# Optimization experiments

Measured on AMD Instinct MI355X. Metric: run time of the kernel, lower is better.

The kernel has to match this reference:

```python
import jax, jax.numpy as jnp
import numpy as np

B, N, C, K, T = 64, 1024, 256, 512, 64
D_THRESH = 0.5
POWER_ITERS = 20


def _pdist(x):
    # x: [..., K, 3] -> pairwise euclidean distances [..., K, K]
    n = jnp.sum(x * x, axis=-1)
    sq = n[..., :, None] + n[..., None, :] - 2.0 * jnp.einsum('...kc,...lc->...kl', x, x)
    return jnp.sqrt(jnp.maximum(sq, 0.0) + 1e-12)


def _forward(rt, rt_centroids, rt_cls_attn, shift_and_scale, W_in, b_in, W1, b1, W2, b2,
             num_rt, anc_idx, pos_idx, neg_idx):
    valid = jnp.arange(N)[None, :] < num_rt[:, None]                      # [B,N]
    # Normalize.batch_unnormalize: pts * scale + shift on valid tokens
    shift = shift_and_scale[:, None, :3]
    scale = shift_and_scale[:, None, 3:4]
    cent = jnp.where(valid[..., None], rt_centroids * scale + shift, rt_centroids)
    attn = jnp.where(valid, rt_cls_attn, -1e9)
    _, top_idx = jax.lax.top_k(attn, K)                                   # [B,K]
    cent_k = jnp.take_along_axis(cent, top_idx[..., None], axis=1)        # [B,K,3]
    rt_k = jnp.take_along_axis(rt, top_idx[..., None], axis=1)            # [B,K,C]
    # SGV padding mask [T,2,K,K]: rows masked by anchor count, cols by pos/neg counts
    n_eff = jnp.minimum(num_rt, K)
    r = jnp.arange(K)
    row_mask = r[None, :] < n_eff[anc_idx][:, None]                       # [T,K]
    col_mask = jnp.stack([r[None, :] < n_eff[pos_idx][:, None],
                          r[None, :] < n_eff[neg_idx][:, None]], axis=1)  # [T,2,K]
    mask = row_mask[:, None, :, None] & col_mask[:, :, None, :]           # [T,2,K,K]
    # input_linear on anchor / neighbour relay tokens
    anc_f = rt_k[anc_idx] @ W_in + b_in                                   # [T,K,C]
    nn_f = jnp.stack([rt_k[pos_idx], rt_k[neg_idx]], axis=1) @ W_in + b_in  # [T,2,K,C]
    anc_c = cent_k[anc_idx]                                               # [T,K,3]
    nn_c = jnp.stack([cent_k[pos_idx], cent_k[neg_idx]], axis=1)          # [T,2,K,3]
    # feature-space nearest-neighbour correspondences anc -> nn (SpectralGV style)
    fd = (jnp.sum(anc_f ** 2, -1)[:, None, :, None]
          + jnp.sum(nn_f ** 2, -1)[:, :, None, :]
          - 2.0 * jnp.einsum('tkc,tnlc->tnkl', anc_f, nn_f))              # [T,2,K,K]
    corr = jnp.argmin(fd, axis=-1)                                        # [T,2,K]
    q_c = jnp.take_along_axis(nn_c, corr[..., None], axis=2)              # [T,2,K,3]
    q_f = jnp.take_along_axis(nn_f, corr[..., None], axis=2)              # [T,2,K,C]
    # correspondence confidence from feature cosine similarity
    cos = jnp.sum(anc_f[:, None] * q_f, -1) / (
        jnp.linalg.norm(anc_f, axis=-1)[:, None] * jnp.linalg.norm(q_f, axis=-1) + 1e-8)
    s = jax.nn.relu(cos)                                                  # [T,2,K]
    # threshold-masked geometric consistency adjacency
    d_p = _pdist(anc_c)[:, None]                                          # [T,1,K,K]
    d_q = _pdist(q_c)                                                     # [T,2,K,K]
    geo = (jnp.abs(d_p - d_q) < D_THRESH) & mask & (~jnp.eye(K, dtype=bool))
    A = geo.astype(jnp.float32) * s[..., :, None] * s[..., None, :]       # [T,2,K,K]
    # leading eigenvector via power iteration (A is entrywise nonnegative)
    v = jnp.full((T, 2, K), 1.0 / np.sqrt(K), dtype=jnp.float32)
    for _ in range(POWER_ITERS):
        w = jnp.einsum('tnkl,tnl->tnk', A, v)
        v = w / (jnp.linalg.norm(w, axis=-1, keepdims=True) + 1e-8)
    eig = -jnp.sort(-v, axis=-1)                                          # sort_eigvec, descending
    h = jax.nn.relu(eig @ W1 + b1)
    scores = jax.nn.sigmoid(h @ W2 + b2)                                  # [T,2,1]
    targets = jnp.zeros_like(scores).at[:, 0].set(1.0)
    return scores, targets


def setup_inputs() -> dict:
    key = jax.random.key(0)
    ks = jax.random.split(key, 12)
    return {
        'rt': jax.random.normal(ks[0], (B, N, C), jnp.float32),
        'rt_centroids': jax.random.normal(ks[1], (B, N, 3), jnp.float32),
        'rt_cls_attn': jax.random.uniform(ks[2], (B, N), jnp.float32),
        'shift_and_scale': jax.random.uniform(ks[3], (B, 4), jnp.float32),
        'num_rt': jax.random.randint(ks[4], (B,), 128, N, jnp.int32),
        'anc_idx': jax.random.randint(ks[5], (T,), 0, B, jnp.int32),
        'pos_idx': jax.random.randint(ks[6], (T,), 0, B, jnp.int32),
        'neg_idx': jax.random.randint(ks[7], (T,), 0, B, jnp.int32),
        'W_in': jax.random.normal(ks[8], (C, C), jnp.float32) / np.sqrt(C),
        'b_in': jnp.zeros((C,), jnp.float32),
        'W1': jax.random.normal(ks[9], (K, K), jnp.float32) / np.sqrt(K),
        'b1': jnp.zeros((K,), jnp.float32),
        'W2': jax.random.normal(ks[10], (K, 1), jnp.float32) / np.sqrt(K),
        'b2': jnp.zeros((1,), jnp.float32),
    }


def reference(rt, rt_centroids, rt_cls_attn, shift_and_scale, num_rt, anc_idx, pos_idx, neg_idx,
              W_in, b_in, W1, b1, W2, b2):
    return _forward(rt, rt_centroids, rt_cls_attn, shift_and_scale, W_in, b_in, W1, b1, W2, b2,
                    num_rt, anc_idx, pos_idx, neg_idx)
```

## Files before the change

### kernel.cpp

```cpp
#include <hip/hip_runtime.h>
#include <cstddef>

#define BB 64
#define NN 1024
#define CC 256
#define KK 512
#define TT 64
#define NPAIR 128

typedef _Float16 h8 __attribute__((ext_vector_type(8)));
typedef _Float16 h4 __attribute__((ext_vector_type(4)));
typedef float f4 __attribute__((ext_vector_type(4)));

typedef __attribute__((address_space(1))) const void GV;
typedef __attribute__((address_space(3))) void LV;
#define GLDS16(g, s) __builtin_amdgcn_global_load_lds((GV*)(const void*)(g), (LV*)(void*)(s), 16, 0, 0)


__global__ __launch_bounds__(256) void wtrans_kernel(
    const float* __restrict__ Win, _Float16* __restrict__ wth, _Float16* __restrict__ wtl)
{
    __shared__ float t[64][65];
    const int k0 = blockIdx.x * 64, n0 = blockIdx.y * 64;
    const int tid = threadIdx.x;
    const int c = tid & 63, r0 = tid >> 6;
    for (int r = r0; r < 64; r += 4)
        t[r][c] = Win[(size_t)(k0 + r) * CC + n0 + c];
    __syncthreads();
    for (int r = r0; r < 64; r += 4) {
        float x = t[c][r];
        _Float16 h = (_Float16)x;
        size_t o = (size_t)(n0 + r) * CC + k0 + c;
        wth[o] = h;
        wtl[o] = (_Float16)(x - (float)h);
    }
}

__global__ __launch_bounds__(512) void sel_kernel(
    const float* __restrict__ attn, const float* __restrict__ cents,
    const float* __restrict__ sas, const int* __restrict__ num_rt,
    int* __restrict__ topidx, int* __restrict__ neff, float* __restrict__ centk)
{
    __shared__ unsigned long long keys[1024];
    const int b = blockIdx.x, tid = threadIdx.x;
    const int nr = num_rt[b];
    for (int i = tid; i < 1024; i += 512) {
        float a = (i < nr) ? attn[b * NN + i] : -1e9f;
        unsigned u = __float_as_uint(a);
        u = (u & 0x80000000u) ? ~u : (u | 0x80000000u);
        keys[i] = ((unsigned long long)u << 32) | (unsigned)(0xFFFFFFFFu - (unsigned)i);
    }
    __syncthreads();
    for (int k = 2; k <= 1024; k <<= 1) {
        for (int j = k >> 1; j > 0; j >>= 1) {
            int i = ((tid & ~(j - 1)) << 1) | (tid & (j - 1));
            int p = i | j;
            unsigned long long a = keys[i], c = keys[p];
            bool up = (i & k) == 0;
            if (up ? (a < c) : (a > c)) { keys[i] = c; keys[p] = a; }
            __syncthreads();
        }
    }
    {
        unsigned long long key = keys[tid];
        int idx = (int)(~(unsigned)key);
        float x = cents[(b * NN + idx) * 3 + 0];
        float y = cents[(b * NN + idx) * 3 + 1];
        float z = cents[(b * NN + idx) * 3 + 2];
        if (idx < nr) {
            float sc = sas[b * 4 + 3];
            x = x * sc + sas[b * 4 + 0];
            y = y * sc + sas[b * 4 + 1];
            z = z * sc + sas[b * 4 + 2];
        }
        float nc = x * x + y * y + z * z;
        ((float4*)centk)[b * KK + tid] = make_float4(x, y, z, nc);
        topidx[b * KK + tid] = idx;
    }
    if (tid == 0) neff[b] = (nr < KK) ? nr : KK;
}

__global__ __launch_bounds__(256) void feat_mfma(
    const float* __restrict__ rt, const int* __restrict__ topidx,
    const _Float16* __restrict__ wth, const _Float16* __restrict__ wtl,
    const float* __restrict__ bin,
    _Float16* __restrict__ feath, _Float16* __restrict__ featl)
{
    const int mtile = blockIdx.x, nt = blockIdx.y;
    __shared__ _Float16 Ah[128][32], Al[128][32], Bh[128][32], Bl[128][32];
    __shared__ int tix[128];
    const int tid = threadIdx.x;
    const int w = tid >> 6, lane = tid & 63;
    const int quad = lane >> 4, l16 = lane & 15;
    const int wm = (w >> 1) * 64, wl = (w & 1) * 64;
    const int b = mtile >> 2;
    if (tid < 128) tix[tid] = topidx[mtile * 128 + tid];
    __syncthreads();
    const int arow_i = tid >> 1;
    const int aseg = (tid & 1) * 16;
    const float* arow = rt + ((size_t)b * NN + tix[arow_i]) * CC + aseg;
    _Float16* bsh = (w < 2) ? &Bh[0][0] : &Bl[0][0];
    const _Float16* bplane = (w < 2) ? wth : wtl;
    const int rowi = lane >> 2, chunk = lane & 3;

    f4 acc[4][4];
    #pragma unroll
    for (int i = 0; i < 4; i++)
        #pragma unroll
        for (int j = 0; j < 4; j++)
            acc[i][j] = (f4){0.f, 0.f, 0.f, 0.f};

    for (int k0 = 0; k0 < CC; k0 += 32) {
        __syncthreads();
        #pragma unroll
        for (int jj = 0; jj < 4; jj++) {
            int j = (w & 1) * 4 + jj;
            int row = j * 16 + rowi;
            GLDS16(bplane + (size_t)(nt * 128 + row) * CC + k0 + chunk * 8, bsh + j * 512);
        }
        {
            const float4* src = (const float4*)(arow + k0);
            #pragma unroll
            for (int c = 0; c < 2; c++) {
                float4 p = src[2 * c], q2 = src[2 * c + 1];
                float xv[8] = {p.x, p.y, p.z, p.w, q2.x, q2.y, q2.z, q2.w};
                h8 hv, lv;
                #pragma unroll
                for (int j = 0; j < 8; j++) {
                    _Float16 h = (_Float16)xv[j];
                    hv[j] = h;
                    lv[j] = (_Float16)(xv[j] - (float)h);
                }
                *(h8*)&Ah[arow_i][aseg + c * 8] = hv;
                *(h8*)&Al[arow_i][aseg + c * 8] = lv;
            }
        }
        __syncthreads();
        h8 afh[4], afl[4], bfh[4], bfl[4];
        #pragma unroll
        for (int i = 0; i < 4; i++) {
            int ra = wm + i * 16 + l16;
            int rb = wl + i * 16 + l16;
            afh[i] = *(const h8*)&Ah[ra][quad * 8];
            afl[i] = *(const h8*)&Al[ra][quad * 8];
            bfh[i] = *(const h8*)&Bh[rb][quad * 8];
            bfl[i] = *(const h8*)&Bl[rb][quad * 8];
        }
        #pragma unroll
        for (int i = 0; i < 4; i++)
            #pragma unroll
            for (int j = 0; j < 4; j++) {
                acc[i][j] = __builtin_amdgcn_mfma_f32_16x16x32_f16(afh[i], bfh[j], acc[i][j], 0, 0, 0);
                acc[i][j] = __builtin_amdgcn_mfma_f32_16x16x32_f16(afh[i], bfl[j], acc[i][j], 0, 0, 0);
                acc[i][j] = __builtin_amdgcn_mfma_f32_16x16x32_f16(afl[i], bfh[j], acc[i][j], 0, 0, 0);
            }
    }
    #pragma unroll
    for (int j = 0; j < 4; j++) {
        int col = wl + j * 16 + l16;
        float bj = bin[nt * 128 + col];
        #pragma unroll
        for (int i = 0; i < 4; i++)
            #pragma unroll
            for (int r = 0; r < 4; r++) {
                int row = wm + i * 16 + quad * 4 + r;
                float v = acc[i][j][r] + bj;
                _Float16 h = (_Float16)v;
                size_t o = (size_t)(mtile * 128 + row) * CC + nt * 128 + col;
                feath[o] = h;
                featl[o] = (_Float16)(v - (float)h);
            }
    }
}

__global__ __launch_bounds__(256) void norm_kernel(
    const _Float16* __restrict__ feath, const _Float16* __restrict__ featl,
    float* __restrict__ normF)
{
    int r = blockIdx.x * 4 + (threadIdx.x >> 6);
    int lane = threadIdx.x & 63;
    h4 hv = ((const h4*)(feath + (size_t)r * CC))[lane];
    h4 lv = ((const h4*)(featl + (size_t)r * CC))[lane];
    float s = 0.f;
    #pragma unroll
    for (int j = 0; j < 4; j++) {
        float x = (float)hv[j] + (float)lv[j];
        s += x * x;
    }
    for (int off = 32; off; off >>= 1) s += __shfl_down(s, off);
    if (lane == 0) normF[r] = s;
}

__global__ __launch_bounds__(512) void argmin_mfma(
    const _Float16* __restrict__ feath, const _Float16* __restrict__ featl,
    const float* __restrict__ normF,
    const int* __restrict__ anc, const int* __restrict__ pos, const int* __restrict__ neg,
    float* __restrict__ partv, int* __restrict__ partl, float* __restrict__ partd)
{
    const int id = blockIdx.x;
    const int xcd = id & 7, kgrp = id >> 3;
    const int pr = xcd * 16 + (kgrp >> 2);
    const int s = kgrp & 3;
    const int lt = s & 1, kt = s >> 1;
    const int t = pr >> 1, nn2 = pr & 1;
    const int a = anc[t];
    const int bb = nn2 ? neg[t] : pos[t];
    const size_t Abase = ((size_t)a * KK + kt * 256) * CC;
    const size_t Bbase = ((size_t)bb * KK + lt * 256) * CC;
    __shared__ _Float16 S[2][4][8192];
    __shared__ float rdv[256][2];
    __shared__ int   rdl[256][2];
    __shared__ float rdd[256][2];
    const int tid = threadIdx.x;
    const int w = tid >> 6, lane = tid & 63;
    const int quad = lane >> 4, l16 = lane & 15;
    const int wr = w >> 1, wc = w & 1;
    const int rowi = lane >> 2, chunk = lane & 3;
    const int plane = w >> 1;
    const int srow = (w & 1) * 128;
    const _Float16* gsrc = (plane == 0) ? feath + Abase
                         : (plane == 1) ? featl + Abase
                         : (plane == 2) ? feath + Bbase
                         :                featl + Bbase;
    const _Float16* grow = gsrc + (size_t)(srow + rowi) * CC + chunk * 8;

    f4 acc[4][8];
    #pragma unroll
    for (int i = 0; i < 4; i++)
        #pragma unroll
        for (int j = 0; j < 8; j++)
            acc[i][j] = (f4){0.f, 0.f, 0.f, 0.f};

    #pragma unroll
    for (int j = 0; j < 8; j++)
        GLDS16(grow + (size_t)(j * 16) * CC, &S[0][plane][srow * 32 + j * 512]);

    #pragma unroll
    for (int kk = 0; kk < 8; kk++) {
        const int cb = kk & 1;
        if (kk < 7) {
            const int k1 = (kk + 1) * 32;
            #pragma unroll
            for (int j = 0; j < 8; j++)
                GLDS16(grow + (size_t)(j * 16) * CC + k1, &S[cb ^ 1][plane][srow * 32 + j * 512]);
            asm volatile("s_waitcnt vmcnt(8)" ::: "memory");
        } else {
            asm volatile("s_waitcnt vmcnt(0)" ::: "memory");
        }
        __builtin_amdgcn_s_barrier();
        h8 afh[4], afl[4];
        #pragma unroll
        for (int i = 0; i < 4; i++) {
            int ra = wr * 64 + i * 16 + l16;
            afh[i] = *(const h8*)&S[cb][0][ra * 32 + quad * 8];
            afl[i] = *(const h8*)&S[cb][1][ra * 32 + quad * 8];
        }
        #pragma unroll
        for (int j = 0; j < 8; j++) {
            int rb = wc * 128 + j * 16 + l16;
            h8 bfh = *(const h8*)&S[cb][2][rb * 32 + quad * 8];
            h8 bfl = *(const h8*)&S[cb][3][rb * 32 + quad * 8];
            #pragma unroll
            for (int i = 0; i < 4; i++) {
                acc[i][j] = __builtin_amdgcn_mfma_f32_16x16x32_f16(afh[i], bfh, acc[i][j], 0, 0, 0);
                acc[i][j] = __builtin_amdgcn_mfma_f32_16x16x32_f16(afh[i], bfl, acc[i][j], 0, 0, 0);
                acc[i][j] = __builtin_amdgcn_mfma_f32_16x16x32_f16(afl[i], bfh, acc[i][j], 0, 0, 0);
            }
        }
        __builtin_amdgcn_sched_barrier(0);
        __builtin_amdgcn_s_barrier();
    }
    float nbj[8];
    #pragma unroll
    for (int j = 0; j < 8; j++)
        nbj[j] = normF[(size_t)bb * KK + lt * 256 + wc * 128 + j * 16 + l16];
    #pragma unroll
    for (int i = 0; i < 4; i++) {
        #pragma unroll
        for (int r = 0; r < 4; r++) {
            float bv = INFINITY; int bl = 0; float bd = 0.f;
            #pragma unroll
            for (int j = 0; j < 8; j++) {
                float d = acc[i][j][r];
                float v = nbj[j] - 2.f * d;
                int l = lt * 256 + wc * 128 + j * 16 + l16;
                if (v < bv) { bv = v; bl = l; bd = d; }
            }
            #pragma unroll
            for (int off = 1; off < 16; off <<= 1) {
                float ov = __shfl_xor(bv, off);
                int   ol = __shfl_xor(bl, off);
                float od = __shfl_xor(bd, off);
                if (ov < bv || (ov == bv && ol < bl)) { bv = ov; bl = ol; bd = od; }
            }
            if (l16 == 0) {
                int row = wr * 64 + i * 16 + quad * 4 + r;
                rdv[row][wc] = bv;
                rdl[row][wc] = bl;
                rdd[row][wc] = bd;
            }
        }
    }
    __syncthreads();
    if (tid < 256) {
        float bv = rdv[tid][0]; int bl = rdl[tid][0]; float bd = rdd[tid][0];
        float v1 = rdv[tid][1]; int l1 = rdl[tid][1];
        if (v1 < bv || (v1 == bv && l1 < bl)) { bv = v1; bl = l1; bd = rdd[tid][1]; }
        size_t idx = ((size_t)pr * KK + kt * 256 + tid) * 2 + lt;
        partv[idx] = bv; partl[idx] = bl; partd[idx] = bd;
    }
}

__global__ __launch_bounds__(256) void geo_kernel(
    const float* __restrict__ centk,
    const float* __restrict__ partv, const int* __restrict__ partl,
    const float* __restrict__ partd, const float* __restrict__ normF,
    const int* __restrict__ neff,
    const int* __restrict__ anc, const int* __restrict__ pos, const int* __restrict__ neg,
    float* __restrict__ sbuf, unsigned* __restrict__ gmask)
{
    const int kt = blockIdx.x;
    const int lt4 = blockIdx.y;
    const int pair = blockIdx.z;
    const int t = pair >> 1, nn2 = pair & 1;
    const int a = anc[t];
    const int bb2 = (nn2 == 0) ? pos[t] : neg[t];
    const int nea = neff[a], neb = neff[bb2];
    const bool writer = (kt == 0) && (lt4 == 0);
    __shared__ int ci[512];
    __shared__ __align__(16) float4 ca[512], cq[512];
    for (int i = threadIdx.x; i < KK; i += 256) {
        size_t base = ((size_t)pair * KK + i) * 2;
        float bv = partv[base]; int bl = partl[base]; float bd = partd[base];
        float v = partv[base + 1]; int l = partl[base + 1];
        if (v < bv || (v == bv && l < bl)) { bv = v; bl = l; bd = partd[base + 1]; }
        ci[i] = bl;
        if (writer) {
            float na = normF[(size_t)a * KK + i];
            float nb = normF[(size_t)bb2 * KK + bl];
            float cosv = bd / (sqrtf(na) * sqrtf(nb) + 1e-8f);
            sbuf[pair * KK + i] = fmaxf(cosv, 0.f);
        }
    }
    __syncthreads();
    for (int i = threadIdx.x; i < KK; i += 256) {
        ca[i] = ((const float4*)centk)[a * KK + i];
        cq[i] = ((const float4*)centk)[bb2 * KK + ci[i]];
    }
    __syncthreads();
    const int k = kt * 256 + threadIdx.x;
    float4 pk = ca[k], qk = cq[k];
    bool rowm = k < nea;
    unsigned* outp = gmask + ((size_t)pair * KK + k) * 16 + lt4 * 4;
    for (int w = 0; w < 4; w++) {
        unsigned word = 0;
        #pragma unroll
        for (int bi = 0; bi < 32; bi++) {
            int l = lt4 * 128 + w * 32 + bi;
            float4 pl = ca[l], ql = cq[l];
            float dp2 = pk.w + pl.w - 2.f * (pk.x * pl.x + pk.y * pl.y + pk.z * pl.z);
            float dp = sqrtf(fmaxf(dp2, 0.f) + 1e-12f);
            float dq2 = qk.w + ql.w - 2.f * (qk.x * ql.x + qk.y * ql.y + qk.z * ql.z);
            float dq = sqrtf(fmaxf(dq2, 0.f) + 1e-12f);
            bool g = (fabsf(dp - dq) < 0.5f) && rowm && (l < neb) && (l != k);
            word |= (g ? (1u << bi) : 0u);
        }
        outp[w] = word;
    }
}

__global__ __launch_bounds__(1024, 4) void power_kernel(
    const unsigned* __restrict__ gmask, const float* __restrict__ sbuf,
    const int* __restrict__ neff,
    const int* __restrict__ anc, const int* __restrict__ pos, const int* __restrict__ neg,
    const float* __restrict__ W1, const float* __restrict__ b1,
    const float* __restrict__ W2, const float* __restrict__ b2,
    float* __restrict__ out)
{
    const int pair = blockIdx.x;
    const int tid = threadIdx.x;
    const int row = tid & 511;
    const int half = tid >> 9;
    const int tt = pair >> 1, nn2 = pair & 1;
    const int a = anc[tt];
    const int bb2 = (nn2 == 0) ? pos[tt] : neg[tt];
    const int nea = neff[a], neb = neff[bb2];
    __shared__ __align__(16) float u[512];
    __shared__ float T[64][257];
    __shared__ float pacc[1024];
    __shared__ float red[16];
    __shared__ float ev[512];
    __shared__ float hpart[1024];
    unsigned m[8];
    const unsigned* g = gmask + ((size_t)pair * KK + row) * 16 + half * 8;
    #pragma unroll
    for (int w = 0; w < 8; w++) m[w] = g[w];
    const float s = sbuf[pair * KK + row];
    const bool arow = (row < nea);
    int nw = (neb - half * 256 + 31) >> 5;
    nw = (nw < 0) ? 0 : (nw > 8 ? 8 : nw);
    const int bp = tid & 63;
    const int vh = tid >> 6;
    const int GV_[16] = {0,1,3,2,6,7,5,4,12,13,15,14,10,11,9,8};
    const int GB[15] = {0,1,0,2,0,1,0,3,0,1,0,2,0,1,0};
    const float GS[15] = {1.f,1.f,-1.f,1.f,1.f,-1.f,-1.f,1.f,1.f,1.f,-1.f,-1.f,1.f,-1.f,-1.f};
    float v = 0.044194173824159216f;
    if (half == 0) u[row] = s * v;
    __syncthreads();
    for (int it = 0; it < 20; it++) {
        {
            float4 ulo = *(const float4*)&u[bp * 8];
            float4 uhi = *(const float4*)&u[bp * 8 + 4];
            float ul[4] = {ulo.x, ulo.y, ulo.z, ulo.w};
            float H = 0.f;
            H += (float)((vh >> 0) & 1) * uhi.x;
            H += (float)((vh >> 1) & 1) * uhi.y;
            H += (float)((vh >> 2) & 1) * uhi.z;
            H += (float)((vh >> 3) & 1) * uhi.w;
            float L = 0.f;
            T[bp][vh * 16 + 0] = H;
            #pragma unroll
            for (int k = 1; k < 16; k++) {
                L += GS[k - 1] * ul[GB[k - 1]];
                T[bp][vh * 16 + GV_[k]] = H + L;
            }
        }
        __syncthreads();
        float a0 = 0.f, a1 = 0.f, a2 = 0.f, a3 = 0.f;
        if (arow) {
            for (int w = 0; w < nw; w++) {
                unsigned mw = m[w];
                const int p0 = half * 32 + w * 4;
                a0 += T[p0 + 0][mw & 255u];
                a1 += T[p0 + 1][(mw >> 8) & 255u];
                a2 += T[p0 + 2][(mw >> 16) & 255u];
                a3 += T[p0 + 3][mw >> 24];
            }
        }
        pacc[tid] = (a0 + a1) + (a2 + a3);
        __syncthreads();
        float wk = s * (pacc[row] + pacc[row + 512]);
        if ((it & 3) == 3) {
            float t2 = wk * wk;
            for (int off = 32; off; off >>= 1) t2 += __shfl_down(t2, off);
            if ((tid & 63) == 0) red[tid >> 6] = t2;
            __syncthreads();
            float tot = 0.f;
            #pragma unroll
            for (int x = 0; x < 16; x++) tot += red[x];
            tot *= 0.5f;
            v = wk / (sqrtf(tot) + 1e-8f);
            if (half == 0) u[row] = s * v;
            __syncthreads();
        } else {
            if (half == 0) u[row] = s * wk;
            __syncthreads();
        }
    }
    if (half == 0) ev[row] = v;
    __syncthreads();
    for (int kk = 2; kk <= 512; kk <<= 1) {
        for (int j = kk >> 1; j; j >>= 1) {
            if (tid < 256) {
                int i = ((tid & ~(j - 1)) << 1) | (tid & (j - 1));
                int p = i | j;
                float x = ev[i], y = ev[p];
                bool up = (i & kk) == 0;
                if (up ? (x < y) : (x > y)) { ev[i] = y; ev[p] = x; }
            }
            __syncthreads();
        }
    }
    const int cbase = half * 256;
    float h = (half == 0) ? b1[row] : 0.f;
    #pragma unroll 8
    for (int l = 0; l < 256; l++)
        h += ev[cbase + l] * W1[(size_t)(cbase + l) * KK + row];
    hpart[tid] = h;
    __syncthreads();
    float term = 0.f;
    if (half == 0) {
        float hv = fmaxf(hpart[row] + hpart[row + 512], 0.f);
        term = hv * W2[row];
    }
    for (int off = 32; off; off >>= 1) term += __shfl_down(term, off);
    if ((tid & 63) == 0) red[tid >> 6] = term;
    __syncthreads();
    if (tid == 0) {
        float sc = 0.f;
        #pragma unroll
        for (int x = 0; x < 16; x++) sc += red[x];
        sc += b2[0];
        out[pair] = 1.f / (1.f + expf(-sc));
        out[NPAIR + pair] = (pair & 1) ? 0.f : 1.f;
    }
}

extern "C" void kernel_launch(void* const* d_in, const int* in_sizes, int n_in,
                              void* d_out, int out_size, void* d_ws, size_t ws_size,
                              hipStream_t stream) {
    (void)in_sizes; (void)n_in; (void)out_size; (void)ws_size;
    const float* rt    = (const float*)d_in[0];
    const float* cents = (const float*)d_in[1];
    const float* attn  = (const float*)d_in[2];
    const float* sas   = (const float*)d_in[3];
    const int* num_rt  = (const int*)d_in[4];
    const int* anc     = (const int*)d_in[5];
    const int* pos     = (const int*)d_in[6];
    const int* neg     = (const int*)d_in[7];
    const float* Win   = (const float*)d_in[8];
    const float* bin   = (const float*)d_in[9];
    const float* W1    = (const float*)d_in[10];
    const float* b1    = (const float*)d_in[11];
    const float* W2    = (const float*)d_in[12];
    const float* b2    = (const float*)d_in[13];

    float* ws = (float*)d_ws;
    _Float16* feath = (_Float16*)ws;
    _Float16* featl = (_Float16*)(ws + 4194304);
    float* normF = ws + 8388608;
    float* centk = ws + 8421376;
    float* sbuf  = ws + 8552448;
    int* topidx  = (int*)(ws + 8617984);
    int* neffp   = (int*)(ws + 8650752);
    unsigned* gmask = (unsigned*)(ws + 8716352);
    _Float16* wth = (_Float16*)(ws + 8716352 + 786432);
    _Float16* wtl = (_Float16*)(ws + 8716352 + 819200);
    float* partv = (float*)(ws + 9764928);
    int*   partl = (int*)(ws + 10027072);
    float* partd = (float*)(ws + 10289216);
    float* out = (float*)d_out;

    wtrans_kernel<<<dim3(4, 4), 256, 0, stream>>>(Win, wth, wtl);
    sel_kernel<<<64, 512, 0, stream>>>(attn, cents, sas, num_rt, topidx, neffp, centk);
    feat_mfma<<<dim3(256, 2), 256, 0, stream>>>(rt, topidx, wth, wtl, bin, feath, featl);
    norm_kernel<<<8192, 256, 0, stream>>>(feath, featl, normF);
    argmin_mfma<<<512, 512, 0, stream>>>(feath, featl, normF, anc, pos, neg, partv, partl, partd);
    geo_kernel<<<dim3(2, 4, 128), 256, 0, stream>>>(centk, partv, partl, partd, normF, neffp, anc, pos, neg, sbuf, gmask);
    power_kernel<<<128, 1024, 0, stream>>>(gmask, sbuf, neffp, anc, pos, neg, W1, b1, W2, b2, out);
}
```

Baseline: 347.2 us.

## Add power-iteration early exit, skip zero-score rows, stream mask words from global

The power-iteration loop now stops early when the normalized vector is bit-identical to the previous normalized iterate, checked every fourth iteration through a shared flag. Rows whose score is zero skip the table-lookup accumulation. Mask words are loaded from global memory with a one-ahead prefetch instead of being held in registers, which lowers register pressure but adds global reads on every iteration. The u vector is stored in a permuted LDS layout so the table-build reads are contiguous float4 loads. Exact-equality convergence rarely triggers with float rounding, so the early exit may seldom save work.

Result: slower. 379.4 us (+9.3%).

```diff
diff --git a/kernel.cpp b/kernel.cpp
--- a/kernel.cpp
+++ b/kernel.cpp
@@ -385,32 +385,32 @@
     const int a = anc[tt];
     const int bb2 = (nn2 == 0) ? pos[tt] : neg[tt];
     const int nea = neff[a], neb = neff[bb2];
-    __shared__ __align__(16) float u[512];
+    __shared__ __align__(16) float uu[512];
     __shared__ float T[64][257];
     __shared__ float pacc[1024];
     __shared__ float red[16];
     __shared__ float ev[512];
     __shared__ float hpart[1024];
-    unsigned m[8];
-    const unsigned* g = gmask + ((size_t)pair * KK + row) * 16 + half * 8;
-    #pragma unroll
-    for (int w = 0; w < 8; w++) m[w] = g[w];
+    __shared__ int convflag;
+    const unsigned* gm = gmask + ((size_t)pair * KK + row) * 16 + half * 8;
     const float s = sbuf[pair * KK + row];
     const bool arow = (row < nea);
     int nw = (neb - half * 256 + 31) >> 5;
     nw = (nw < 0) ? 0 : (nw > 8 ? 8 : nw);
     const int bp = tid & 63;
     const int vh = tid >> 6;
+    #define UADDR(r) ((((r) & 4) << 6) + (((r) >> 3) << 2) + ((r) & 3))
     const int GV_[16] = {0,1,3,2,6,7,5,4,12,13,15,14,10,11,9,8};
     const int GB[15] = {0,1,0,2,0,1,0,3,0,1,0,2,0,1,0};
     const float GS[15] = {1.f,1.f,-1.f,1.f,1.f,-1.f,-1.f,1.f,1.f,1.f,-1.f,-1.f,1.f,-1.f,-1.f};
     float v = 0.044194173824159216f;
-    if (half == 0) u[row] = s * v;
+    float vnprev = v;
+    if (half == 0) uu[UADDR(row)] = s * v;
     __syncthreads();
     for (int it = 0; it < 20; it++) {
         {
-            float4 ulo = *(const float4*)&u[bp * 8];
-            float4 uhi = *(const float4*)&u[bp * 8 + 4];
+            float4 ulo = *(const float4*)&uu[bp * 4];
+            float4 uhi = *(const float4*)&uu[256 + bp * 4];
             float ul[4] = {ulo.x, ulo.y, ulo.z, ulo.w};
             float H = 0.f;
             H += (float)((vh >> 0) & 1) * uhi.x;
@@ -427,14 +427,16 @@
         }
         __syncthreads();
         float a0 = 0.f, a1 = 0.f, a2 = 0.f, a3 = 0.f;
-        if (arow) {
-            for (int w = 0; w < nw; w++) {
-                unsigned mw = m[w];
+        if (arow && s != 0.f) {
+            unsigned mw = (nw > 0) ? gm[0] : 0u;
+            for (int w = 0; w < nw; ++w) {
+                unsigned nx = (w + 1 < nw) ? gm[w + 1] : 0u;
                 const int p0 = half * 32 + w * 4;
                 a0 += T[p0 + 0][mw & 255u];
                 a1 += T[p0 + 1][(mw >> 8) & 255u];
                 a2 += T[p0 + 2][(mw >> 16) & 255u];
                 a3 += T[p0 + 3][mw >> 24];
+                mw = nx;
             }
         }
         pacc[tid] = (a0 + a1) + (a2 + a3);
@@ -444,16 +446,21 @@
             float t2 = wk * wk;
             for (int off = 32; off; off >>= 1) t2 += __shfl_down(t2, off);
             if ((tid & 63) == 0) red[tid >> 6] = t2;
+            if (tid == 0) convflag = 1;
             __syncthreads();
             float tot = 0.f;
             #pragma unroll
             for (int x = 0; x < 16; x++) tot += red[x];
             tot *= 0.5f;
             v = wk / (sqrtf(tot) + 1e-8f);
-            if (half == 0) u[row] = s * v;
+            bool eq = (__float_as_uint(v) == __float_as_uint(vnprev));
+            vnprev = v;
+            if (half == 0) uu[UADDR(row)] = s * v;
+            if (!eq) convflag = 0;
             __syncthreads();
+            if (convflag) break;
         } else {
-            if (half == 0) u[row] = s * wk;
+            if (half == 0) uu[UADDR(row)] = s * wk;
             __syncthreads();
         }
     }
```
